# Optimization experiments

Measured on AMD Instinct MI355X. Metric: run time of the kernel, lower is better.

## Reference

```python
import jax, jax.numpy as jnp
import numpy as np

N_ATOMS = 25000
N_PAIRS = 500000
C = 64        # pp_nodes[-1] == ii_nodes[-1]
PI_N = 32     # pi_nodes[-1]
NB = 8        # n_basis
N_PROPS = 2   # rank//2 + 1 for rank=3


def setup_inputs() -> dict:
    key = jax.random.key(0)
    ks = jax.random.split(key, 16)
    g = lambda k, s, fan: (jax.random.normal(k, s, jnp.float32) / np.float32(np.sqrt(fan)))
    ind_2 = jax.random.randint(ks[0], (N_PAIRS, 2), 0, N_ATOMS, dtype=jnp.int32)
    p1 = jax.random.normal(ks[1], (N_ATOMS, C), jnp.float32)
    p3 = jax.random.normal(ks[2], (N_ATOMS, 3, C), jnp.float32)
    d3 = jax.random.normal(ks[3], (N_PAIRS, 3), jnp.float32)
    basis = jax.random.normal(ks[4], (N_PAIRS, NB), jnp.float32)
    # InvarLayer params
    W_pi = g(ks[5], (2 * C, PI_N * NB), 2 * C)   # PILayer FF (bias, tanh)
    b_pi = jnp.zeros((PI_N * NB,), jnp.float32)
    W_ii = g(ks[6], (PI_N, C * N_PROPS), PI_N)   # ii layer, no bias
    W_pp = g(ks[7], (C * N_PROPS, C), 2 * C)     # pp layer, no bias
    # EquiVarLayer (rank 3) params
    wi_pix = g(ks[8], (C, C), C)
    wj_pix = g(ks[9], (C, C), C)
    W_ppx = g(ks[10], (C, C), C)                 # pp layer: no bias, no activation
    wi_dot = g(ks[11], (C, C), C)
    wj_dot = g(ks[12], (C, C), C)
    # GCBlock final pp layer (bias, tanh)
    W_pp1 = g(ks[13], (2 * C, 2 * C), 2 * C)
    b_pp1 = jnp.zeros((2 * C,), jnp.float32)
    return dict(ind_2=ind_2, p1=p1, p3=p3, d3=d3, basis=basis,
                W_pi=W_pi, b_pi=b_pi, W_ii=W_ii, W_pp=W_pp,
                wi_pix=wi_pix, wj_pix=wj_pix, W_ppx=W_ppx,
                wi_dot=wi_dot, wj_dot=wj_dot, W_pp1=W_pp1, b_pp1=b_pp1)


def reference(ind_2, p1, p3, d3, basis, W_pi, b_pi, W_ii, W_pp,
              wi_pix, wj_pix, W_ppx, wi_dot, wj_dot, W_pp1, b_pp1):
    ii = ind_2[:, 0]
    jj = ind_2[:, 1]
    n_atoms = p1.shape[0]

    # ---- InvarLayer ----
    # PILayer: gather pair endpoints, FF to [P, PI_N*NB], contract with basis
    inter = jnp.concatenate([p1[ii], p1[jj]], axis=-1)         # [P, 2C]
    inter = jnp.tanh(inter @ W_pi + b_pi)                      # [P, PI_N*NB]
    inter = inter.reshape(-1, PI_N, NB)
    i1_pre = jnp.einsum('pcb,pb->pc', inter, basis)            # [P, PI_N]
    # ii FF (no bias)
    i1 = jnp.tanh(i1_pre @ W_ii)                               # [P, 2C]
    # IPLayer: scatter-sum interactions to atoms
    p1_agg = jax.ops.segment_sum(i1, ii, num_segments=n_atoms) # [N, 2C]
    p1_new = jnp.tanh(p1_agg @ W_pp)                           # [N, C]

    i1_0, i1_1 = jnp.split(i1, N_PROPS, axis=-1)               # each [P, C]

    # ---- EquiVarLayer (rank 3) ----
    # weighted PIXLayer: channel-mix gathered endpoint vectors
    ix = (jnp.einsum('pxc,cd->pxd', p3[ii], wi_pix)
          + jnp.einsum('pxc,cd->pxd', p3[jj], wj_pix))         # [P, 3, C]
    # scale(ix, i1) + scale(diff[:, :, None], i1)
    ix = (ix + d3[:, :, None]) * i1_1[:, None, :]              # [P, 3, C]
    p3_agg = jax.ops.segment_sum(ix, ii, num_segments=n_atoms) # [N, 3, C]
    p3_mixed = jnp.einsum('nxc,cd->nxd', p3_agg, W_ppx)        # [N, 3, C]
    # weighted DotLayer: reduce the equivariant axis
    dotted_p3 = jnp.einsum('nxr,nxr->nr',
                           jnp.einsum('nxc,cr->nxr', p3_mixed, wi_dot),
                           jnp.einsum('nxc,cr->nxr', p3_mixed, wj_dot))  # [N, C]

    # ---- GCBlock stitch ----
    p1t1 = jnp.tanh(jnp.concatenate([p1_new, dotted_p3], axis=-1) @ W_pp1 + b_pp1)  # [N, 2C]
    p1_out, s3 = jnp.split(p1t1, N_PROPS, axis=-1)             # each [N, C]
    p3_out = p3_mixed * s3[:, None, :]                         # [N, 3, C]
    return (p1_out, p3_out, dotted_p3, i1, ix)
```

## Files before the change

kernel.cpp:

```cpp
#include <hip/hip_runtime.h>

#define NP 500000
#define NA 25000

__device__ __forceinline__ float tanh_fast(float x) {
    float e = __expf(2.0f * x);
    return 1.0f - 2.0f / (e + 1.0f);
}

__device__ __forceinline__ float readlane_f(float v, int lane) {
    int iv = __builtin_bit_cast(int, v);
    int r = __builtin_amdgcn_readlane(iv, lane);
    return __builtin_bit_cast(float, r);
}

__device__ __forceinline__ float dpp8_reduce(float s) {
    int x;
    x = __builtin_amdgcn_update_dpp(0, __builtin_bit_cast(int, s), 0xB1, 0xF, 0xF, true);
    s += __builtin_bit_cast(float, x);
    x = __builtin_amdgcn_update_dpp(0, __builtin_bit_cast(int, s), 0x4E, 0xF, 0xF, true);
    s += __builtin_bit_cast(float, x);
    x = __builtin_amdgcn_update_dpp(0, __builtin_bit_cast(int, s), 0x141, 0xF, 0xF, true);
    s += __builtin_bit_cast(float, x);
    return s;
}

__device__ __forceinline__ unsigned short f2bf(float x) {
    union { float f; unsigned int u; } c; c.f = x;
    unsigned int r = c.u + 0x7FFFu + ((c.u >> 16) & 1u);
    return (unsigned short)(r >> 16);
}
__device__ __forceinline__ float bf2f(unsigned short h) {
    union { unsigned int u; float f; } c; c.u = ((unsigned int)h) << 16;
    return c.f;
}
__device__ __forceinline__ unsigned int pack2bf(float a, float b) {
    return (unsigned int)f2bf(a) | ((unsigned int)f2bf(b) << 16);
}
__device__ __forceinline__ float lo_bf(unsigned int x) { return bf2f((unsigned short)(x & 0xffffu)); }
__device__ __forceinline__ float hi_bf(unsigned int x) { return bf2f((unsigned short)(x >> 16)); }
__device__ __forceinline__ float lo_bf_f(unsigned int x) {
    return __builtin_bit_cast(float, x << 16);
}
__device__ __forceinline__ float hi_bf_f(unsigned int x) {
    return __builtin_bit_cast(float, x & 0xffff0000u);
}

extern "C" __global__ __launch_bounds__(256, 2)
void k0_uv(const float* __restrict__ p1,
           const float* __restrict__ W_pi,
           const float* __restrict__ b_pi,
           float* __restrict__ u,
           unsigned short* __restrict__ vq)
{
    __shared__ float sW[32 * 256];
    __shared__ float sp1[16 * 64];

    const int t = threadIdx.x;
    const int wv = t >> 6;
    const int l = t & 63;
    const int atom0 = blockIdx.x * 16;

    #pragma unroll
    for (int f = 0; f < 4; ++f) {
        int idx = f * 256 + t;
        int at = atom0 + (idx >> 6);
        int atc = at < NA ? at : NA - 1;
        sp1[idx] = p1[(size_t)atc * 64 + (idx & 63)];
    }

    float accu[4][4] = {{0}}, accv[4][4] = {{0}};

    #pragma unroll
    for (int s = 0; s < 4; ++s) {
        __syncthreads();
        {
            const float4* src = (const float4*)(W_pi + s * 32 * 256);
            float4* dst = (float4*)sW;
            #pragma unroll
            for (int f = 0; f < 8; ++f) dst[f * 256 + t] = src[f * 256 + t];
        }
        __syncthreads();
        const int kbase = (s & 1) * 32;
        #pragma unroll 2
        for (int k = 0; k < 32; ++k) {
            float wq[4];
            #pragma unroll
            for (int q = 0; q < 4; ++q) wq[q] = sW[k * 256 + 64 * q + l];
            #pragma unroll
            for (int a = 0; a < 4; ++a) {
                float pv = sp1[(wv * 4 + a) * 64 + kbase + k];
                #pragma unroll
                for (int q = 0; q < 4; ++q) {
                    if (s < 2) accu[a][q] = fmaf(pv, wq[q], accu[a][q]);
                    else       accv[a][q] = fmaf(pv, wq[q], accv[a][q]);
                }
            }
        }
    }

    #pragma unroll
    for (int a = 0; a < 4; ++a) {
        const int at = atom0 + wv * 4 + a;
        if (at < NA) {
            #pragma unroll
            for (int q = 0; q < 4; ++q)
                u[(size_t)at * 256 + 64 * q + l] = accu[a][q] + b_pi[64 * q + l];
            uint2 vv;
            vv.x = pack2bf(accv[a][0], accv[a][1]);
            vv.y = pack2bf(accv[a][2], accv[a][3]);
            *(uint2*)&vq[(size_t)at * 512 + 8 * l] = vv;
        }
    }
}

extern "C" __global__ __launch_bounds__(256, 4)
void k0_q(const float* __restrict__ p3,
          const float* __restrict__ wi_pix,
          const float* __restrict__ wj_pix,
          unsigned short* __restrict__ qi_bf,
          unsigned short* __restrict__ vq)
{
    __shared__ float sWi[64 * 64];
    __shared__ float sWj[64 * 64];

    const int t = threadIdx.x;
    {
        const float4* si = (const float4*)wi_pix;
        const float4* sj = (const float4*)wj_pix;
        float4* di = (float4*)sWi;
        float4* dj = (float4*)sWj;
        #pragma unroll
        for (int f = 0; f < 4; ++f) { di[f * 256 + t] = si[f * 256 + t]; dj[f * 256 + t] = sj[f * 256 + t]; }
    }
    __syncthreads();

    const int w = t >> 6;
    const int l = t & 63;
    const int atom = blockIdx.x * 4 + w;

    float val0 = p3[((size_t)atom * 3 + 0) * 64 + l];
    float val1 = p3[((size_t)atom * 3 + 1) * 64 + l];
    float val2 = p3[((size_t)atom * 3 + 2) * 64 + l];

    float ai[3] = {0, 0, 0}, aj[3] = {0, 0, 0};
    #pragma unroll 8
    for (int k = 0; k < 64; ++k) {
        float a0 = readlane_f(val0, k);
        float a1 = readlane_f(val1, k);
        float a2 = readlane_f(val2, k);
        float wi = sWi[k * 64 + l];
        float wj = sWj[k * 64 + l];
        ai[0] = fmaf(a0, wi, ai[0]); aj[0] = fmaf(a0, wj, aj[0]);
        ai[1] = fmaf(a1, wi, ai[1]); aj[1] = fmaf(a1, wj, aj[1]);
        ai[2] = fmaf(a2, wi, ai[2]); aj[2] = fmaf(a2, wj, aj[2]);
    }
    uint2 iu, ju;
    iu.x = pack2bf(ai[0], ai[1]); iu.y = pack2bf(ai[2], 0.0f);
    ju.x = pack2bf(aj[0], aj[1]); ju.y = pack2bf(aj[2], 0.0f);
    *(uint2*)&qi_bf[(size_t)atom * 256 + 4 * l] = iu;
    *(uint2*)&vq[(size_t)atom * 512 + 8 * l + 4] = ju;
}

extern "C" __global__ void k_count(const int* __restrict__ ind2, int* __restrict__ cnt)
{
    int p = blockIdx.x * 256 + threadIdx.x;
    if (p < NP) atomicAdd(&cnt[ind2[2 * p]], 1);
}

extern "C" __global__ __launch_bounds__(1024)
void csr_scan(const int* __restrict__ cnt, int* __restrict__ rowstart)
{
    __shared__ int ssum[1024];
    const int t = threadIdx.x;
    const int base = t * 25;

    int s = 0;
    #pragma unroll 5
    for (int i = 0; i < 25; ++i) {
        int idx = base + i;
        s += (idx < NA) ? cnt[idx] : 0;
    }
    ssum[t] = s;
    __syncthreads();
    for (int off = 1; off < 1024; off <<= 1) {
        int vv = (t >= off) ? ssum[t - off] : 0;
        __syncthreads();
        ssum[t] += vv;
        __syncthreads();
    }
    int run = (t > 0) ? ssum[t - 1] : 0;
    for (int i = 0; i < 25; ++i) {
        int idx = base + i;
        if (idx <= NA) rowstart[idx] = run;
        run += (idx < NA) ? cnt[idx] : 0;
    }
}

extern "C" __global__ void k_scatter(const int* __restrict__ ind2,
                                     const int* __restrict__ rowstart,
                                     int* __restrict__ cursor,
                                     int2* __restrict__ plist2)
{
    int p = blockIdx.x * 256 + threadIdx.x;
    if (p < NP) {
        int ii = ind2[2 * p];
        int jj = ind2[2 * p + 1];
        int pos = atomicAdd(&cursor[ii], 1);
        plist2[rowstart[ii] + pos] = make_int2(p, jj);
    }
}

extern "C" __global__ __launch_bounds__(256, 4)
void k_pair(const float* __restrict__ d3,
            const float* __restrict__ basis,
            const float* __restrict__ W_ii,
            const float* __restrict__ u,
            const unsigned short* __restrict__ vq,
            const unsigned short* __restrict__ qi_bf,
            const int* __restrict__ rowstart,
            const int2* __restrict__ plist2,
            float* __restrict__ out_i1,
            float* __restrict__ out_ix,
            float* __restrict__ p1_agg,
            float* __restrict__ p3_agg)
{
    const int t = threadIdx.x;
    const int w = t >> 6;
    const int l = t & 63;
    const int n = blockIdx.x * 4 + w;

    unsigned int wAB[32];
    #pragma unroll
    for (int c = 0; c < 32; ++c)
        wAB[c] = pack2bf(W_ii[c * 128 + l], W_ii[c * 128 + 64 + l]);

    float uu[4];
    #pragma unroll
    for (int q = 0; q < 4; ++q) uu[q] = u[(size_t)n * 256 + 64 * q + l];
    float qiv[3];
    {
        uint2 iu = *(const uint2*)&qi_bf[(size_t)n * 256 + 4 * l];
        qiv[0] = lo_bf(iu.x); qiv[1] = hi_bf(iu.x); qiv[2] = lo_bf(iu.y);
    }

    const int start = rowstart[n];
    const int end   = rowstart[n + 1];

    float agg1a = 0.0f, agg1b = 0.0f;
    float agg30 = 0.0f, agg31 = 0.0f, agg32 = 0.0f;

    if (start < end) {
        const int last = end - 1;

        int2 pjA = plist2[start];
        uint4 vqA = *(const uint4*)&vq[(size_t)pjA.y * 512 + 8 * l];
        float bsA = basis[(size_t)pjA.x * 8 + (l & 7)];
        float dA0 = d3[3 * (size_t)pjA.x + 0];
        float dA1 = d3[3 * (size_t)pjA.x + 1];
        float dA2 = d3[3 * (size_t)pjA.x + 2];

        int iB = (start + 1 <= last) ? start + 1 : last;
        int2 pjB = plist2[iB];
        uint4 vqB = *(const uint4*)&vq[(size_t)pjB.y * 512 + 8 * l];
        float bsB = basis[(size_t)pjB.x * 8 + (l & 7)];
        float dB0 = d3[3 * (size_t)pjB.x + 0];
        float dB1 = d3[3 * (size_t)pjB.x + 1];
        float dB2 = d3[3 * (size_t)pjB.x + 2];

        int iC = (start + 2 <= last) ? start + 2 : last;
        int2 pjC = plist2[iC];

        for (int it = start; it < end; ++it) {
            uint4 vqC = *(const uint4*)&vq[(size_t)pjC.y * 512 + 8 * l];
            float bsC = basis[(size_t)pjC.x * 8 + (l & 7)];
            float dC0 = d3[3 * (size_t)pjC.x + 0];
            float dC1 = d3[3 * (size_t)pjC.x + 1];
            float dC2 = d3[3 * (size_t)pjC.x + 2];
            int iD = (it + 3 <= last) ? it + 3 : last;
            int2 pjD = plist2[iD];

            float hq0 = tanh_fast(uu[0] + lo_bf(vqA.x));
            float hq1 = tanh_fast(uu[1] + hi_bf(vqA.x));
            float hq2 = tanh_fast(uu[2] + lo_bf(vqA.y));
            float hq3 = tanh_fast(uu[3] + hi_bf(vqA.y));

            float pre[4];
            pre[0] = dpp8_reduce(hq0 * bsA);
            pre[1] = dpp8_reduce(hq1 * bsA);
            pre[2] = dpp8_reduce(hq2 * bsA);
            pre[3] = dpp8_reduce(hq3 * bsA);

            float a00 = 0, a01 = 0, a10 = 0, a11 = 0;
            #pragma unroll
            for (int c = 0; c < 32; c += 2) {
                float p0 = readlane_f(pre[c >> 3], 8 * (c & 7));
                float p1 = readlane_f(pre[(c + 1) >> 3], 8 * ((c + 1) & 7));
                a00 = fmaf(p0, lo_bf_f(wAB[c]), a00);
                a10 = fmaf(p0, hi_bf_f(wAB[c]), a10);
                a01 = fmaf(p1, lo_bf_f(wAB[c + 1]), a01);
                a11 = fmaf(p1, hi_bf_f(wAB[c + 1]), a11);
            }
            const float i10 = tanh_fast(a00 + a01);
            const float i11 = tanh_fast(a10 + a11);

            const size_t pA = (size_t)pjA.x;
            __builtin_nontemporal_store(i10, &out_i1[pA * 128 + l]);
            __builtin_nontemporal_store(i11, &out_i1[pA * 128 + 64 + l]);
            agg1a += i10;
            agg1b += i11;

            float ix0 = (qiv[0] + lo_bf(vqA.z) + dA0) * i11;
            float ix1 = (qiv[1] + hi_bf(vqA.z) + dA1) * i11;
            float ix2 = (qiv[2] + lo_bf(vqA.w) + dA2) * i11;
            __builtin_nontemporal_store(ix0, &out_ix[(pA * 3 + 0) * 64 + l]);
            __builtin_nontemporal_store(ix1, &out_ix[(pA * 3 + 1) * 64 + l]);
            __builtin_nontemporal_store(ix2, &out_ix[(pA * 3 + 2) * 64 + l]);
            agg30 += ix0; agg31 += ix1; agg32 += ix2;

            pjA = pjB; vqA = vqB; bsA = bsB; dA0 = dB0; dA1 = dB1; dA2 = dB2;
            pjB = pjC; vqB = vqC; bsB = bsC; dB0 = dC0; dB1 = dC1; dB2 = dC2;
            pjC = pjD;
        }
    }

    p1_agg[(size_t)n * 128 + l]      = agg1a;
    p1_agg[(size_t)n * 128 + 64 + l] = agg1b;
    p3_agg[(size_t)n * 192 + l]       = agg30;
    p3_agg[(size_t)n * 192 + 64 + l]  = agg31;
    p3_agg[(size_t)n * 192 + 128 + l] = agg32;
}

extern "C" __global__ __launch_bounds__(256, 4)
void k3_atoms(const float* __restrict__ p1_agg,
              const float* __restrict__ p3_agg,
              const float* __restrict__ W_pp,
              const float* __restrict__ W_ppx,
              const float* __restrict__ wi_dot,
              const float* __restrict__ wj_dot,
              const float* __restrict__ W_pp1,
              const float* __restrict__ b_pp1,
              float* __restrict__ out_p1,
              float* __restrict__ out_p3,
              float* __restrict__ out_dot)
{
    __shared__ float s1[4][128];
    __shared__ float s3[4][192];
    __shared__ float sPm[4][192];
    __shared__ float sCat[4][128];

    const int w = threadIdx.x >> 6;
    const int l = threadIdx.x & 63;
    const int n = blockIdx.x * 4 + w;

    s1[w][l]      = p1_agg[(size_t)n * 128 + l];
    s1[w][64 + l] = p1_agg[(size_t)n * 128 + 64 + l];
    #pragma unroll
    for (int x = 0; x < 3; ++x)
        s3[w][x * 64 + l] = p3_agg[(size_t)n * 192 + x * 64 + l];
    __syncthreads();

    float pn = 0.0f;
    #pragma unroll 4
    for (int k = 0; k < 128; ++k)
        pn = fmaf(s1[w][k], W_pp[k * 64 + l], pn);
    pn = tanh_fast(pn);

    float pm[3];
    #pragma unroll
    for (int x = 0; x < 3; ++x) {
        float s = 0.0f;
        #pragma unroll 4
        for (int c = 0; c < 64; ++c)
            s = fmaf(s3[w][x * 64 + c], W_ppx[c * 64 + l], s);
        pm[x] = s;
        sPm[w][x * 64 + l] = s;
    }
    __syncthreads();

    float dot = 0.0f;
    #pragma unroll
    for (int x = 0; x < 3; ++x) {
        float vi = 0.0f, vj = 0.0f;
        #pragma unroll 4
        for (int c = 0; c < 64; ++c) {
            float a = sPm[w][x * 64 + c];
            vi = fmaf(a, wi_dot[c * 64 + l], vi);
            vj = fmaf(a, wj_dot[c * 64 + l], vj);
        }
        dot = fmaf(vi, vj, dot);
    }

    sCat[w][l]      = pn;
    sCat[w][64 + l] = dot;
    __syncthreads();

    float u1 = b_pp1[l];
    float u2 = b_pp1[64 + l];
    #pragma unroll 4
    for (int k = 0; k < 128; ++k) {
        float ck = sCat[w][k];
        u1 = fmaf(ck, W_pp1[k * 128 + l], u1);
        u2 = fmaf(ck, W_pp1[k * 128 + 64 + l], u2);
    }
    float p1o = tanh_fast(u1);
    float s3v = tanh_fast(u2);

    out_p1[(size_t)n * 64 + l]  = p1o;
    out_dot[(size_t)n * 64 + l] = dot;
    #pragma unroll
    for (int x = 0; x < 3; ++x)
        out_p3[((size_t)n * 3 + x) * 64 + l] = pm[x] * s3v;
}

extern "C" void kernel_launch(void* const* d_in, const int* in_sizes, int n_in,
                              void* d_out, int out_size, void* d_ws, size_t ws_size,
                              hipStream_t stream)
{
    const int*   ind2   = (const int*)d_in[0];
    const float* p1     = (const float*)d_in[1];
    const float* p3     = (const float*)d_in[2];
    const float* d3     = (const float*)d_in[3];
    const float* basis  = (const float*)d_in[4];
    const float* W_pi   = (const float*)d_in[5];
    const float* b_pi   = (const float*)d_in[6];
    const float* W_ii   = (const float*)d_in[7];
    const float* W_pp   = (const float*)d_in[8];
    const float* wi_pix = (const float*)d_in[9];
    const float* wj_pix = (const float*)d_in[10];
    const float* W_ppx  = (const float*)d_in[11];
    const float* wi_dot = (const float*)d_in[12];
    const float* wj_dot = (const float*)d_in[13];
    const float* W_pp1  = (const float*)d_in[14];
    const float* b_pp1  = (const float*)d_in[15];

    float* out     = (float*)d_out;
    float* out_p1  = out;
    float* out_p3  = out + 1600000;
    float* out_dot = out + 6400000;
    float* out_i1  = out + 8000000;
    float* out_ix  = out + 72000000;

    float*          u      = (float*)d_ws;
    unsigned short* vq     = (unsigned short*)(u + 6400000);
    unsigned short* qi_bf  = vq + 12800000;
    float*          p1_agg = (float*)(qi_bf + 6400000);
    float*          p3_agg = p1_agg + 3200000;
    int2*           plist2 = (int2*)(p3_agg + 4800000);
    int*            cnt      = (int*)(plist2 + 500000);
    int*            rowstart = cnt + 25000;
    int*            cursor   = rowstart + 25001;

    hipMemsetAsync(cnt, 0, (size_t)75001 * sizeof(int), stream);

    dim3 blk(256);
    k0_uv    <<<dim3(1563), blk, 0, stream>>>(p1, W_pi, b_pi, u, vq);
    k0_q     <<<dim3(6250), blk, 0, stream>>>(p3, wi_pix, wj_pix, qi_bf, vq);
    k_count  <<<dim3(1954), blk, 0, stream>>>(ind2, cnt);
    csr_scan <<<dim3(1), dim3(1024), 0, stream>>>(cnt, rowstart);
    k_scatter<<<dim3(1954), blk, 0, stream>>>(ind2, rowstart, cursor, plist2);
    k_pair   <<<dim3(6250), blk, 0, stream>>>(d3, basis, W_ii, u, vq,
                                              qi_bf, rowstart, plist2,
                                              out_i1, out_ix, p1_agg, p3_agg);
    k3_atoms <<<dim3(6250), blk, 0, stream>>>(p1_agg, p3_agg, W_pp, W_ppx,
                                              wi_dot, wj_dot, W_pp1, b_pp1,
                                              out_p1, out_p3, out_dot);
}
```

Measured before the change: 602.9 us.

## Fuse pair counting into k0_q and process two pairs per iteration in k_pair

The separate k_count launch is removed, and its atomic histogram of ii indices now runs at the start of k0_q, whose 6250×256 threads cover all pairs. The per-pair loop in k_pair now handles two pairs per iteration with interleaved tanh, DPP reductions and readlane FMAs, which exposes more independent work and prefetches the next two pairs' gathers together. This saves one kernel launch and adds ILP to hide latency, at the cost of higher register pressure and a guarded tail for odd pair counts.

```diff
diff --git a/kernel.cpp b/kernel.cpp
--- a/kernel.cpp
+++ b/kernel.cpp
@@ -118,6 +118,8 @@
 void k0_q(const float* __restrict__ p3,
           const float* __restrict__ wi_pix,
           const float* __restrict__ wj_pix,
+          const int* __restrict__ ind2,
+          int* __restrict__ cnt,
           unsigned short* __restrict__ qi_bf,
           unsigned short* __restrict__ vq)
 {
@@ -125,6 +127,12 @@
     __shared__ float sWj[64 * 64];
 
     const int t = threadIdx.x;
+
+    {
+        int gp = blockIdx.x * 256 + t;
+        if (gp < NP) atomicAdd(&cnt[ind2[2 * gp]], 1);
+    }
+
     {
         const float4* si = (const float4*)wi_pix;
         const float4* sj = (const float4*)wj_pix;
@@ -160,12 +168,6 @@
     ju.x = pack2bf(aj[0], aj[1]); ju.y = pack2bf(aj[2], 0.0f);
     *(uint2*)&qi_bf[(size_t)atom * 256 + 4 * l] = iu;
     *(uint2*)&vq[(size_t)atom * 512 + 8 * l + 4] = ju;
-}
-
-extern "C" __global__ void k_count(const int* __restrict__ ind2, int* __restrict__ cnt)
-{
-    int p = blockIdx.x * 256 + threadIdx.x;
-    if (p < NP) atomicAdd(&cnt[ind2[2 * p]], 1);
 }
 
 extern "C" __global__ __launch_bounds__(1024)
@@ -253,74 +255,110 @@
     if (start < end) {
         const int last = end - 1;
 
-        int2 pjA = plist2[start];
-        uint4 vqA = *(const uint4*)&vq[(size_t)pjA.y * 512 + 8 * l];
-        float bsA = basis[(size_t)pjA.x * 8 + (l & 7)];
-        float dA0 = d3[3 * (size_t)pjA.x + 0];
-        float dA1 = d3[3 * (size_t)pjA.x + 1];
-        float dA2 = d3[3 * (size_t)pjA.x + 2];
-
-        int iB = (start + 1 <= last) ? start + 1 : last;
-        int2 pjB = plist2[iB];
-        uint4 vqB = *(const uint4*)&vq[(size_t)pjB.y * 512 + 8 * l];
-        float bsB = basis[(size_t)pjB.x * 8 + (l & 7)];
-        float dB0 = d3[3 * (size_t)pjB.x + 0];
-        float dB1 = d3[3 * (size_t)pjB.x + 1];
-        float dB2 = d3[3 * (size_t)pjB.x + 2];
-
-        int iC = (start + 2 <= last) ? start + 2 : last;
-        int2 pjC = plist2[iC];
-
-        for (int it = start; it < end; ++it) {
-            uint4 vqC = *(const uint4*)&vq[(size_t)pjC.y * 512 + 8 * l];
-            float bsC = basis[(size_t)pjC.x * 8 + (l & 7)];
-            float dC0 = d3[3 * (size_t)pjC.x + 0];
-            float dC1 = d3[3 * (size_t)pjC.x + 1];
-            float dC2 = d3[3 * (size_t)pjC.x + 2];
+        int2 pj0, pj1;
+        uint4 vq0, vq1;
+        float bs0, bs1;
+        float d0x, d0y, d0z, d1x, d1y, d1z;
+
+        {
+            int iA = start;
+            int iB = (start + 1 <= last) ? start + 1 : last;
+            pj0 = plist2[iA];
+            pj1 = plist2[iB];
+            vq0 = *(const uint4*)&vq[(size_t)pj0.y * 512 + 8 * l];
+            vq1 = *(const uint4*)&vq[(size_t)pj1.y * 512 + 8 * l];
+            bs0 = basis[(size_t)pj0.x * 8 + (l & 7)];
+            bs1 = basis[(size_t)pj1.x * 8 + (l & 7)];
+            d0x = d3[3 * (size_t)pj0.x + 0]; d0y = d3[3 * (size_t)pj0.x + 1]; d0z = d3[3 * (size_t)pj0.x + 2];
+            d1x = d3[3 * (size_t)pj1.x + 0]; d1y = d3[3 * (size_t)pj1.x + 1]; d1z = d3[3 * (size_t)pj1.x + 2];
+        }
+
+        for (int it = start; it < end; it += 2) {
+            int iC = (it + 2 <= last) ? it + 2 : last;
             int iD = (it + 3 <= last) ? it + 3 : last;
-            int2 pjD = plist2[iD];
-
-            float hq0 = tanh_fast(uu[0] + lo_bf(vqA.x));
-            float hq1 = tanh_fast(uu[1] + hi_bf(vqA.x));
-            float hq2 = tanh_fast(uu[2] + lo_bf(vqA.y));
-            float hq3 = tanh_fast(uu[3] + hi_bf(vqA.y));
-
-            float pre[4];
-            pre[0] = dpp8_reduce(hq0 * bsA);
-            pre[1] = dpp8_reduce(hq1 * bsA);
-            pre[2] = dpp8_reduce(hq2 * bsA);
-            pre[3] = dpp8_reduce(hq3 * bsA);
-
-            float a00 = 0, a01 = 0, a10 = 0, a11 = 0;
+            int2 pjT0 = plist2[iC];
+            int2 pjT1 = plist2[iD];
+            uint4 vqT0 = *(const uint4*)&vq[(size_t)pjT0.y * 512 + 8 * l];
+            uint4 vqT1 = *(const uint4*)&vq[(size_t)pjT1.y * 512 + 8 * l];
+            float bsT0 = basis[(size_t)pjT0.x * 8 + (l & 7)];
+            float bsT1 = basis[(size_t)pjT1.x * 8 + (l & 7)];
+            float dT0x = d3[3 * (size_t)pjT0.x + 0];
+            float dT0y = d3[3 * (size_t)pjT0.x + 1];
+            float dT0z = d3[3 * (size_t)pjT0.x + 2];
+            float dT1x = d3[3 * (size_t)pjT1.x + 0];
+            float dT1y = d3[3 * (size_t)pjT1.x + 1];
+            float dT1z = d3[3 * (size_t)pjT1.x + 2];
+
+            float h00 = tanh_fast(uu[0] + lo_bf(vq0.x));
+            float h10 = tanh_fast(uu[0] + lo_bf(vq1.x));
+            float h01 = tanh_fast(uu[1] + hi_bf(vq0.x));
+            float h11 = tanh_fast(uu[1] + hi_bf(vq1.x));
+            float h02 = tanh_fast(uu[2] + lo_bf(vq0.y));
+            float h12 = tanh_fast(uu[2] + lo_bf(vq1.y));
+            float h03 = tanh_fast(uu[3] + hi_bf(vq0.y));
+            float h13 = tanh_fast(uu[3] + hi_bf(vq1.y));
+
+            float pre0[4], pre1[4];
+            pre0[0] = dpp8_reduce(h00 * bs0);
+            pre1[0] = dpp8_reduce(h10 * bs1);
+            pre0[1] = dpp8_reduce(h01 * bs0);
+            pre1[1] = dpp8_reduce(h11 * bs1);
+            pre0[2] = dpp8_reduce(h02 * bs0);
+            pre1[2] = dpp8_reduce(h12 * bs1);
+            pre0[3] = dpp8_reduce(h03 * bs0);
+            pre1[3] = dpp8_reduce(h13 * bs1);
+
+            float a0A = 0, a0B = 0, a1A = 0, a1B = 0;
+            float b0A = 0, b0B = 0, b1A = 0, b1B = 0;
             #pragma unroll
             for (int c = 0; c < 32; c += 2) {
-                float p0 = readlane_f(pre[c >> 3], 8 * (c & 7));
-                float p1 = readlane_f(pre[(c + 1) >> 3], 8 * ((c + 1) & 7));
-                a00 = fmaf(p0, lo_bf_f(wAB[c]), a00);
-                a10 = fmaf(p0, hi_bf_f(wAB[c]), a10);
-                a01 = fmaf(p1, lo_bf_f(wAB[c + 1]), a01);
-                a11 = fmaf(p1, hi_bf_f(wAB[c + 1]), a11);
+                float p00 = readlane_f(pre0[c >> 3], 8 * (c & 7));
+                float p10 = readlane_f(pre1[c >> 3], 8 * (c & 7));
+                float p01 = readlane_f(pre0[(c + 1) >> 3], 8 * ((c + 1) & 7));
+                float p11 = readlane_f(pre1[(c + 1) >> 3], 8 * ((c + 1) & 7));
+                float wlo0 = lo_bf_f(wAB[c]), whi0 = hi_bf_f(wAB[c]);
+                float wlo1 = lo_bf_f(wAB[c + 1]), whi1 = hi_bf_f(wAB[c + 1]);
+                a0A = fmaf(p00, wlo0, a0A);  b0A = fmaf(p00, whi0, b0A);
+                a1A = fmaf(p10, wlo0, a1A);  b1A = fmaf(p10, whi0, b1A);
+                a0B = fmaf(p01, wlo1, a0B);  b0B = fmaf(p01, whi1, b0B);
+                a1B = fmaf(p11, wlo1, a1B);  b1B = fmaf(p11, whi1, b1B);
             }
-            const float i10 = tanh_fast(a00 + a01);
-            const float i11 = tanh_fast(a10 + a11);
-
-            const size_t pA = (size_t)pjA.x;
-            __builtin_nontemporal_store(i10, &out_i1[pA * 128 + l]);
-            __builtin_nontemporal_store(i11, &out_i1[pA * 128 + 64 + l]);
-            agg1a += i10;
-            agg1b += i11;
-
-            float ix0 = (qiv[0] + lo_bf(vqA.z) + dA0) * i11;
-            float ix1 = (qiv[1] + hi_bf(vqA.z) + dA1) * i11;
-            float ix2 = (qiv[2] + lo_bf(vqA.w) + dA2) * i11;
-            __builtin_nontemporal_store(ix0, &out_ix[(pA * 3 + 0) * 64 + l]);
-            __builtin_nontemporal_store(ix1, &out_ix[(pA * 3 + 1) * 64 + l]);
-            __builtin_nontemporal_store(ix2, &out_ix[(pA * 3 + 2) * 64 + l]);
-            agg30 += ix0; agg31 += ix1; agg32 += ix2;
-
-            pjA = pjB; vqA = vqB; bsA = bsB; dA0 = dB0; dA1 = dB1; dA2 = dB2;
-            pjB = pjC; vqB = vqC; bsB = bsC; dB0 = dC0; dB1 = dC1; dB2 = dC2;
-            pjC = pjD;
+            const float i10_0 = tanh_fast(a0A + a0B);
+            const float i11_0 = tanh_fast(b0A + b0B);
+            const float i10_1 = tanh_fast(a1A + a1B);
+            const float i11_1 = tanh_fast(b1A + b1B);
+
+            {
+                const size_t pA = (size_t)pj0.x;
+                __builtin_nontemporal_store(i10_0, &out_i1[pA * 128 + l]);
+                __builtin_nontemporal_store(i11_0, &out_i1[pA * 128 + 64 + l]);
+                agg1a += i10_0;
+                agg1b += i11_0;
+                float ix0 = (qiv[0] + lo_bf(vq0.z) + d0x) * i11_0;
+                float ix1 = (qiv[1] + hi_bf(vq0.z) + d0y) * i11_0;
+                float ix2 = (qiv[2] + lo_bf(vq0.w) + d0z) * i11_0;
+                __builtin_nontemporal_store(ix0, &out_ix[(pA * 3 + 0) * 64 + l]);
+                __builtin_nontemporal_store(ix1, &out_ix[(pA * 3 + 1) * 64 + l]);
+                __builtin_nontemporal_store(ix2, &out_ix[(pA * 3 + 2) * 64 + l]);
+                agg30 += ix0; agg31 += ix1; agg32 += ix2;
+            }
+            if (it + 1 < end) {
+                const size_t pA = (size_t)pj1.x;
+                __builtin_nontemporal_store(i10_1, &out_i1[pA * 128 + l]);
+                __builtin_nontemporal_store(i11_1, &out_i1[pA * 128 + 64 + l]);
+                agg1a += i10_1;
+                agg1b += i11_1;
+                float ix0 = (qiv[0] + lo_bf(vq1.z) + d1x) * i11_1;
+                float ix1 = (qiv[1] + hi_bf(vq1.z) + d1y) * i11_1;
+                float ix2 = (qiv[2] + lo_bf(vq1.w) + d1z) * i11_1;
+                __builtin_nontemporal_store(ix0, &out_ix[(pA * 3 + 0) * 64 + l]);
+                __builtin_nontemporal_store(ix1, &out_ix[(pA * 3 + 1) * 64 + l]);
+                __builtin_nontemporal_store(ix2, &out_ix[(pA * 3 + 2) * 64 + l]);
+                agg30 += ix0; agg31 += ix1; agg32 += ix2;
+            }
+
+            pj0 = pjT0; vq0 = vqT0; bs0 = bsT0; d0x = dT0x; d0y = dT0y; d0z = dT0z;
+            pj1 = pjT1; vq1 = vqT1; bs1 = bsT1; d1x = dT1x; d1y = dT1y; d1z = dT1z;
         }
     }
 
@@ -455,8 +493,8 @@
 
     dim3 blk(256);
     k0_uv    <<<dim3(1563), blk, 0, stream>>>(p1, W_pi, b_pi, u, vq);
-    k0_q     <<<dim3(6250), blk, 0, stream>>>(p3, wi_pix, wj_pix, qi_bf, vq);
-    k_count  <<<dim3(1954), blk, 0, stream>>>(ind2, cnt);
+    k0_q     <<<dim3(6250), blk, 0, stream>>>(p3, wi_pix, wj_pix, ind2, cnt,
+                                              qi_bf, vq);
     csr_scan <<<dim3(1), dim3(1024), 0, stream>>>(cnt, rowstart);
     k_scatter<<<dim3(1954), blk, 0, stream>>>(ind2, rowstart, cursor, plist2);
     k_pair   <<<dim3(6250), blk, 0, stream>>>(d3, basis, W_ii, u, vq,
```

After: 590.3 us. 1.02x faster.
